# Kernel optimization log

Hardware: AMD Instinct MI355X
Metric: run time of the kernel (lower is better)

## Reference

```python
import jax, jax.numpy as jnp
import numpy as np

B, S, HID = 1, 4096, 1024
NH, HD = 16, 64            # heads, per-head dim
BS = 256                    # block size
PB = 256                    # position buckets (= max_relative_positions)
EPS = 1e-7


def make_log_bucket_position(rel, num_buckets, max_position):
    sign = jnp.sign(rel)
    max_exact = num_buckets // 2
    in_exact = (rel < max_exact) & (rel > -max_exact)
    abs_pos = jnp.where(in_exact, max_exact - 1, jnp.abs(rel))
    x = jnp.log((max_position - 1) / max_exact)
    xx = jnp.log(abs_pos / max_exact) / x
    log_pos = jnp.ceil(xx * (max_exact - 1)) + max_exact
    return jnp.where(abs_pos <= max_exact, rel, (log_pos * sign).astype(jnp.int32)).astype(jnp.int32)


def split_into_blocks(x, block_size, axis):
    # [..., S, ...] -> [..., S//bs, bs, ...]; S assumed divisible by bs
    shp = x.shape
    new = shp[:axis] + (shp[axis] // block_size, block_size) + shp[axis + 1:]
    return x.reshape(new)


def concat_3_blocks(x, block_axis, seq_axis, pad_value=0):
    # pad one zero block on each side of the block axis, then concat
    # [prev, cur, next] along the within-block seq axis.
    pad = [(0, 0)] * x.ndim
    pad[block_axis] = (1, 1)
    xp = jnp.pad(x, pad, constant_values=pad_value)
    nb = x.shape[block_axis]
    slices = [jax.lax.dynamic_slice_in_dim(xp, i, nb, block_axis) for i in range(3)]
    return jnp.concatenate(slices, axis=seq_axis)


def layer_norm(x, scale, bias):
    mu = jnp.mean(x, axis=-1, keepdims=True)
    var = jnp.mean(jnp.square(x - mu), axis=-1, keepdims=True)
    return (x - mu) * jax.lax.rsqrt(var + EPS) * scale + bias


def setup_inputs() -> dict:
    key = jax.random.key(0)
    ks = jax.random.split(key, 8)
    d = {
        'hidden_states': jax.random.normal(ks[0], (B, S, HID), jnp.float32) * 0.02,
        'rel_pos_embeddings': jax.random.normal(ks[1], (S, HID), jnp.float32) * 0.02,
        'Wq': jax.random.normal(ks[2], (HID, HID), jnp.float32) * 0.01,
        'bq': jnp.zeros((HID,), jnp.float32),
        'Wk': jax.random.normal(ks[3], (HID, HID), jnp.float32) * 0.01,
        'bk': jnp.zeros((HID,), jnp.float32),
        'Wv': jax.random.normal(ks[4], (HID, HID), jnp.float32) * 0.01,
        'bv': jnp.zeros((HID,), jnp.float32),
        'Wo': jax.random.normal(ks[5], (HID, HID), jnp.float32) * 0.01,
        'bo': jnp.zeros((HID,), jnp.float32),
        'ln_scale': jnp.ones((HID,), jnp.float32),
        'ln_bias': jnp.zeros((HID,), jnp.float32),
    }
    return d


def reference(hidden_states, rel_pos_embeddings, Wq, bq, Wk, bk, Wv, bv, Wo, bo, ln_scale, ln_bias):
    b, s, hid = hidden_states.shape

    def heads(x):
        return x.reshape(x.shape[:-1] + (NH, HD))

    # content projections -> [B, nb, bs, h, d]
    q = split_into_blocks(heads(hidden_states @ Wq + bq), BS, axis=1)
    k = split_into_blocks(heads(hidden_states @ Wk + bk), BS, axis=1)
    v = split_into_blocks(heads(hidden_states @ Wv + bv), BS, axis=1)
    k3 = concat_3_blocks(k, block_axis=1, seq_axis=2)   # [B, nb, 3bs, h, d]
    v3 = concat_3_blocks(v, block_axis=1, seq_axis=2)

    c2c = jnp.einsum('bnqhd,bnkhd->bnhqk', q, k3)

    # position projections, stacked over batch (size-1 batch dim broadcasts in einsum)
    pos_q = split_into_blocks(heads(rel_pos_embeddings @ Wq + bq)[None], BS, axis=1)  # [1, nb, bs, h, d]
    pos_k = split_into_blocks(heads(rel_pos_embeddings @ Wk + bk)[None], BS, axis=1)
    pos_k3 = concat_3_blocks(pos_k, block_axis=1, seq_axis=2)                          # [1, nb, 3bs, h, d]

    rel = jnp.arange(BS, dtype=jnp.int32)[:, None] - jnp.arange(3 * BS, dtype=jnp.int32)[None, :]
    rel = make_log_bucket_position(rel, PB, PB)
    idx = jnp.clip(rel + PB, 0, 2 * PB - 1)            # [bs, 3bs]

    c2p = jnp.einsum('bnqhd,bnkhd->bnhqk', q, pos_k3)  # [B, nb, h, bs, 3bs]
    # faithful to the source: axis-less jnp.take gathers from the FLATTENED
    # score tensor -> [bs, 3bs] bias broadcast over (batch, block, head)
    c2p_bias = jnp.take(c2p, idx)

    p2c = jnp.einsum('bnqhd,bnkhd->bnhqk', pos_q, k3)
    p2c_bias = jnp.take(p2c, idx)

    scale = jnp.sqrt(jnp.asarray(HD * 3, hidden_states.dtype))
    attn = (c2c + c2p_bias + p2c_bias) / scale
    probs = jax.nn.softmax(attn, axis=-1)

    ctx = jnp.einsum('bnhqk,bnkhd->bnqhd', probs, v3)  # [B, nb, bs, h, d]
    ctx = ctx.reshape(b, s, hid)
    out = ctx @ Wo + bo
    return layer_norm(out + hidden_states, ln_scale, ln_bias)
```

## Files before the change

kernel.cpp:

```cpp
#include <hip/hip_runtime.h>
#include <stdint.h>

typedef unsigned short u16;
typedef __bf16 bf16_t;
typedef bf16_t v8bf __attribute__((ext_vector_type(8)));
typedef float v4f __attribute__((ext_vector_type(4)));

#define SEQ   4096
#define HIDN  1024
#define NHEAD 16
#define HDIM  64
#define BLK   256
#define NBLK  16

#define GLOAD_LDS16(g, l) __builtin_amdgcn_global_load_lds( \
  (const __attribute__((address_space(1))) unsigned*)(g), \
  (__attribute__((address_space(3))) unsigned*)(l), 16, 0, 0)

__device__ __forceinline__ u16 f2bf(float f){
  union { float f; unsigned u; } v; v.f = f;
  unsigned r = (v.u + 0x7fffu + ((v.u >> 16) & 1u)) >> 16;
  return (u16)r;
}
__device__ __forceinline__ float bf2f(u16 h){
  union { unsigned u; float f; } v; v.u = ((unsigned)h) << 16;
  return v.f;
}

__global__ __launch_bounds__(256) void k_prep(const float* __restrict__ hidden, u16* __restrict__ hb,
    const float* __restrict__ Wq, const float* __restrict__ Wk,
    const float* __restrict__ Wv, const float* __restrict__ Wo, u16* __restrict__ Wt,
    const float* __restrict__ bq, const float* __restrict__ bk, const float* __restrict__ bv,
    float* __restrict__ bcat,
    const float* __restrict__ rpe, float* __restrict__ posk, float* __restrict__ posq0)
{
  __shared__ float t[32][33];
  __shared__ float red[4][64];
  int b = blockIdx.x, tid = threadIdx.x;
  if (b < 4096){
    int w = b >> 10, tile = b & 1023;
    int k0 = (tile & 31) * 32, n0 = (tile >> 5) * 32;
    const float* W = (w == 0) ? Wq : (w == 1) ? Wk : (w == 2) ? Wv : Wo;
    u16* outp = Wt + (size_t)w * 1024 * 1024;
    int x = tid & 31, y = tid >> 5;
    #pragma unroll
    for (int yy = 0; yy < 32; yy += 8) t[y + yy][x] = W[(size_t)(k0 + y + yy) * 1024 + n0 + x];
    __syncthreads();
    #pragma unroll
    for (int yy = 0; yy < 32; yy += 8) outp[(size_t)(n0 + y + yy) * 1024 + k0 + x] = f2bf(t[x][y + yy]);
  } else if (b < 4608){
    int base = (b - 4096) * 8192;
    #pragma unroll
    for (int j = 0; j < 8; j++){
      int i = base + j * 1024 + tid * 4;
      float4 f = *(const float4*)&hidden[i];
      unsigned u0 = (unsigned)f2bf(f.x) | ((unsigned)f2bf(f.y) << 16);
      unsigned u1 = (unsigned)f2bf(f.z) | ((unsigned)f2bf(f.w) << 16);
      uint2 p; p.x = u0; p.y = u1;
      *(uint2*)&hb[i] = p;
    }
  } else if (b == 4608){
    #pragma unroll
    for (int j = 0; j < 12; j++){
      int i = j * 256 + tid;
      const float* src = i < 1024 ? bq : (i < 2048 ? bk : bv);
      bcat[i] = src[i & 1023];
    }
  } else {
    int pb = b - 4609;
    int d = tid & 63, part = tid >> 6;
    const float* W  = (pb < 256) ? Wk : Wq;
    const float* rv = (pb < 256) ? &rpe[(size_t)pb * 1024] : rpe;
    float s = 0.f;
    for (int k = part * 256; k < part * 256 + 256; k++) s += rv[k] * W[(size_t)k * 1024 + d];
    red[part][d] = s;
    __syncthreads();
    if (part == 0){
      s = red[0][d] + red[1][d] + red[2][d] + red[3][d];
      if (pb < 256) posk[pb * 64 + d] = s + bk[d];
      else          posq0[d] = s + bq[d];
    }
  }
}

__global__ __launch_bounds__(256) void k_gemm_qkv(const u16* __restrict__ A, const u16* __restrict__ Bt,
                                                  const float* __restrict__ bias,
                                                  u16* __restrict__ qk, u16* __restrict__ Vt)
{
  __shared__ alignas(16) u16 As[2][128 * 32];
  __shared__ alignas(16) u16 Bs[2][128 * 32];
  int tid = threadIdx.x, lane = tid & 63, wid = tid >> 6;
  int wr = wid >> 1, wc = wid & 1;
  int m0 = blockIdx.y * 128, n0 = blockIdx.x * 128;
  const int K = 1024;

  v4f acc[4][4];
  #pragma unroll
  for (int m = 0; m < 4; m++)
    #pragma unroll
    for (int n = 0; n < 4; n++) acc[m][n] = (v4f){0.f, 0.f, 0.f, 0.f};

  int r = lane & 15, g = lane >> 4;
  int ob0 = wid * 2048;
  int o0  = ob0 + lane * 16;
  int row0 = o0 >> 6, col0 = (o0 & 63) >> 1;
  int row1 = (o0 + 1024) >> 6, col1 = ((o0 + 1024) & 63) >> 1;

  GLOAD_LDS16(&A [(size_t)(m0 + row0) * K + col0], &As[0][ob0 >> 1]);
  GLOAD_LDS16(&Bt[(size_t)(n0 + row0) * K + col0], &Bs[0][ob0 >> 1]);
  GLOAD_LDS16(&A [(size_t)(m0 + row1) * K + col1], &As[0][(ob0 + 1024) >> 1]);
  GLOAD_LDS16(&Bt[(size_t)(n0 + row1) * K + col1], &Bs[0][(ob0 + 1024) >> 1]);
  __syncthreads();

  int cur = 0;
  for (int kt = 0; kt < K - 32; kt += 32){
    int nx = cur ^ 1, kn = kt + 32;
    GLOAD_LDS16(&A [(size_t)(m0 + row0) * K + kn + col0], &As[nx][ob0 >> 1]);
    GLOAD_LDS16(&Bt[(size_t)(n0 + row0) * K + kn + col0], &Bs[nx][ob0 >> 1]);
    GLOAD_LDS16(&A [(size_t)(m0 + row1) * K + kn + col1], &As[nx][(ob0 + 1024) >> 1]);
    GLOAD_LDS16(&Bt[(size_t)(n0 + row1) * K + kn + col1], &Bs[nx][(ob0 + 1024) >> 1]);

    v8bf a[4], bb[4];
    #pragma unroll
    for (int m = 0; m < 4; m++) a[m] = *(const v8bf*)&As[cur][(wr * 64 + m * 16 + r) * 32 + g * 8];
    #pragma unroll
    for (int n = 0; n < 4; n++) bb[n] = *(const v8bf*)&Bs[cur][(wc * 64 + n * 16 + r) * 32 + g * 8];
    #pragma unroll
    for (int m = 0; m < 4; m++)
      #pragma unroll
      for (int n = 0; n < 4; n++)
        acc[m][n] = __builtin_amdgcn_mfma_f32_16x16x32_bf16(a[m], bb[n], acc[m][n], 0, 0, 0);
    __syncthreads();
    cur = nx;
  }
  {
    v8bf a[4], bb[4];
    #pragma unroll
    for (int m = 0; m < 4; m++) a[m] = *(const v8bf*)&As[cur][(wr * 64 + m * 16 + r) * 32 + g * 8];
    #pragma unroll
    for (int n = 0; n < 4; n++) bb[n] = *(const v8bf*)&Bs[cur][(wc * 64 + n * 16 + r) * 32 + g * 8];
    #pragma unroll
    for (int m = 0; m < 4; m++)
      #pragma unroll
      for (int n = 0; n < 4; n++)
        acc[m][n] = __builtin_amdgcn_mfma_f32_16x16x32_bf16(a[m], bb[n], acc[m][n], 0, 0, 0);
  }

  #pragma unroll
  for (int m = 0; m < 4; m++)
    #pragma unroll
    for (int n = 0; n < 4; n++){
      int col = n0 + wc * 64 + n * 16 + r;
      float bv = bias[col];
      if (n0 < 2048){
        #pragma unroll
        for (int i = 0; i < 4; i++){
          int row = m0 + wr * 64 + m * 16 + g * 4 + i;
          qk[(size_t)row * 2048 + col] = f2bf(acc[m][n][i] + bv);
        }
      } else {
        unsigned lo = (unsigned)f2bf(acc[m][n][0] + bv) | ((unsigned)f2bf(acc[m][n][1] + bv) << 16);
        unsigned hi = (unsigned)f2bf(acc[m][n][2] + bv) | ((unsigned)f2bf(acc[m][n][3] + bv) << 16);
        uint2 pk; pk.x = lo; pk.y = hi;
        int row = m0 + wr * 64 + m * 16 + g * 4;
        *(uint2*)&Vt[(size_t)(col - 2048) * 4096 + row] = pk;
      }
    }
}

__global__ __launch_bounds__(256) void k_gemm_out(const u16* __restrict__ A, const u16* __restrict__ Bt,
                                                  const float* __restrict__ bias,
                                                  const float* __restrict__ resid, float* __restrict__ Cout)
{
  __shared__ alignas(16) u16 As[2][128 * 32];
  __shared__ alignas(16) u16 Bs[2][128 * 32];
  int tid = threadIdx.x, lane = tid & 63, wid = tid >> 6;
  int wr = wid >> 1, wc = wid & 1;
  int m0 = blockIdx.y * 128, n0 = blockIdx.x * 128;
  const int K = 1024;

  v4f acc[4][4];
  #pragma unroll
  for (int m = 0; m < 4; m++)
    #pragma unroll
    for (int n = 0; n < 4; n++) acc[m][n] = (v4f){0.f, 0.f, 0.f, 0.f};

  int r = lane & 15, g = lane >> 4;
  int ob0 = wid * 2048;
  int o0  = ob0 + lane * 16;
  int row0 = o0 >> 6, col0 = (o0 & 63) >> 1;
  int row1 = (o0 + 1024) >> 6, col1 = ((o0 + 1024) & 63) >> 1;

  GLOAD_LDS16(&A [(size_t)(m0 + row0) * K + col0], &As[0][ob0 >> 1]);
  GLOAD_LDS16(&Bt[(size_t)(n0 + row0) * K + col0], &Bs[0][ob0 >> 1]);
  GLOAD_LDS16(&A [(size_t)(m0 + row1) * K + col1], &As[0][(ob0 + 1024) >> 1]);
  GLOAD_LDS16(&Bt[(size_t)(n0 + row1) * K + col1], &Bs[0][(ob0 + 1024) >> 1]);
  __syncthreads();

  int cur = 0;
  for (int kt = 0; kt < K - 32; kt += 32){
    int nx = cur ^ 1, kn = kt + 32;
    GLOAD_LDS16(&A [(size_t)(m0 + row0) * K + kn + col0], &As[nx][ob0 >> 1]);
    GLOAD_LDS16(&Bt[(size_t)(n0 + row0) * K + kn + col0], &Bs[nx][ob0 >> 1]);
    GLOAD_LDS16(&A [(size_t)(m0 + row1) * K + kn + col1], &As[nx][(ob0 + 1024) >> 1]);
    GLOAD_LDS16(&Bt[(size_t)(n0 + row1) * K + kn + col1], &Bs[nx][(ob0 + 1024) >> 1]);

    v8bf a[4], bb[4];
    #pragma unroll
    for (int m = 0; m < 4; m++) a[m] = *(const v8bf*)&As[cur][(wr * 64 + m * 16 + r) * 32 + g * 8];
    #pragma unroll
    for (int n = 0; n < 4; n++) bb[n] = *(const v8bf*)&Bs[cur][(wc * 64 + n * 16 + r) * 32 + g * 8];
    #pragma unroll
    for (int m = 0; m < 4; m++)
      #pragma unroll
      for (int n = 0; n < 4; n++)
        acc[m][n] = __builtin_amdgcn_mfma_f32_16x16x32_bf16(a[m], bb[n], acc[m][n], 0, 0, 0);
    __syncthreads();
    cur = nx;
  }
  {
    v8bf a[4], bb[4];
    #pragma unroll
    for (int m = 0; m < 4; m++) a[m] = *(const v8bf*)&As[cur][(wr * 64 + m * 16 + r) * 32 + g * 8];
    #pragma unroll
    for (int n = 0; n < 4; n++) bb[n] = *(const v8bf*)&Bs[cur][(wc * 64 + n * 16 + r) * 32 + g * 8];
    #pragma unroll
    for (int m = 0; m < 4; m++)
      #pragma unroll
      for (int n = 0; n < 4; n++)
        acc[m][n] = __builtin_amdgcn_mfma_f32_16x16x32_bf16(a[m], bb[n], acc[m][n], 0, 0, 0);
  }

  #pragma unroll
  for (int m = 0; m < 4; m++)
    #pragma unroll
    for (int n = 0; n < 4; n++){
      int col = n0 + wc * 64 + n * 16 + r;
      float bv = bias[col];
      #pragma unroll
      for (int i = 0; i < 4; i++){
        int row = m0 + wr * 64 + m * 16 + g * 4 + i;
        Cout[(size_t)row * 1024 + col] = acc[m][n][i] + bv + resid[(size_t)row * 1024 + col];
      }
    }
}

__global__ __launch_bounds__(256) void k_brow(const u16* __restrict__ qk,
                                              const float* __restrict__ posk, const float* __restrict__ posq0,
                                              float* __restrict__ brow)
{
  int b = blockIdx.x, tid = threadIdx.x;
  if (tid < 32) brow[b * 32 + tid] = 0.f;
  int u = b * 32 + (tid >> 3), sub = tid & 7;
  float c2p = 0.f, p2c = 0.f;
  #pragma unroll
  for (int j = 0; j < 8; j++){
    int d = sub * 8 + j;
    c2p += bf2f(qk[d]) * posk[u * 64 + d];
    p2c += posq0[d] * bf2f(qk[(size_t)u * 2048 + 1024 + d]);
  }
  float v = c2p + p2c;
  v += __shfl_xor(v, 1);
  v += __shfl_xor(v, 2);
  v += __shfl_xor(v, 4);
  if (sub == 0) brow[256 + u] = v;
}

__global__ void k_biasd(const float* __restrict__ brow, float* __restrict__ biasd)
{
  int t = blockIdx.x * blockDim.x + threadIdx.x;
  int rel = t - 767;
  int bucket;
  bool in_exact = (rel < 128) && (rel > -128);
  int abs_pos = in_exact ? 127 : (rel < 0 ? -rel : rel);
  if (abs_pos <= 128) bucket = rel;
  else {
    float xx = logf((float)abs_pos * (1.0f / 128.0f)) / logf(255.0f / 128.0f);
    float lp = ceilf(xx * 127.0f) + 128.0f;
    int sgn = (rel > 0) ? 1 : ((rel < 0) ? -1 : 0);
    bucket = (int)lp * sgn;
  }
  int idx = bucket + 256;
  idx = idx < 0 ? 0 : (idx > 511 ? 511 : idx);
  biasd[t] = brow[idx];
}

__global__ __launch_bounds__(256) void k_attn(const u16* __restrict__ qk, const u16* __restrict__ Vt,
                                              const float* __restrict__ biasd, u16* __restrict__ ctxg)
{
  __shared__ alignas(16) u16 Ks[128 * 64];
  __shared__ alignas(16) u16 Vs[64 * 128];
  __shared__ alignas(16) u16 Ps[4 * 16 * 128];
  __shared__ float bias_s[1024];

  int b = blockIdx.x;
  int h = b & 15, tile = b >> 4;
  int n = tile >> 2, qb0 = (tile & 3) * 64;
  int tid = threadIdx.x, lane = tid & 63, w = tid >> 6;
  int q0 = tile * 64;
  int g0 = (n - 1) * 256;
  const float c1 = 0.07216878364870323f * 1.4426950408889634f;
  int r = lane & 15, g = lane >> 4;

  *(float4*)&bias_s[tid * 4] = *(const float4*)&biasd[tid * 4];

  v8bf qfrag[2];
  {
    const u16* src = &qk[(size_t)(q0 + w * 16 + r) * 2048 + h * 64 + g * 8];
    qfrag[0] = *(const v8bf*)&src[0];
    qfrag[1] = *(const v8bf*)&src[32];
  }

  u16* Pw = &Ps[w * 2048];
  float m4[4], l4[4];
  v4f pacc[4];
  #pragma unroll
  for (int i = 0; i < 4; i++){ m4[i] = -3.0e38f; l4[i] = 0.f; pacc[i] = (v4f){0.f,0.f,0.f,0.f}; }

  for (int c = 0; c < 6; ++c){
    int cb = g0 + c * 128;
    bool oob = (cb < 0) || (cb >= SEQ);
    if (!oob){
      #pragma unroll
      for (int t = 0; t < 4; ++t){
        int row = w * 32 + t * 8 + (lane >> 3);
        int p = lane & 7;
        GLOAD_LDS16(&qk[(size_t)(cb + row) * 2048 + 1024 + h * 64 + ((p ^ (row & 7)) * 8)],
                    Ks + (size_t)(w * 32 + t * 8) * 64);
      }
      #pragma unroll
      for (int t = 0; t < 4; ++t){
        int d = w * 16 + t * 4 + (lane >> 4);
        int p = lane & 15;
        GLOAD_LDS16(&Vt[(size_t)(h * 64 + d) * 4096 + cb + ((p ^ (d & 7)) * 8)],
                    Vs + (size_t)(w * 16 + t * 4) * 128);
      }
    }
    __syncthreads();

    v4f sacc[8];
    #pragma unroll
    for (int t = 0; t < 8; t++) sacc[t] = (v4f){0.f,0.f,0.f,0.f};
    if (!oob){
      #pragma unroll
      for (int ks = 0; ks < 2; ++ks){
        #pragma unroll
        for (int t = 0; t < 8; t++){
          int kr = t * 16 + r;
          v8bf bb = *(const v8bf*)&Ks[kr * 64 + (((4 * ks + g) ^ (kr & 7)) * 8)];
          sacc[t] = __builtin_amdgcn_mfma_f32_16x16x32_bf16(qfrag[ks], bb, sacc[t], 0, 0, 0);
        }
      }
    }

    float sv[8][4];
    float cm[4] = {-3.0e38f, -3.0e38f, -3.0e38f, -3.0e38f};
    int ib = qb0 + w * 16 + g * 4 + 767 - r - c * 128;
    #pragma unroll
    for (int t = 0; t < 8; t++){
      #pragma unroll
      for (int i = 0; i < 4; i++){
        float s = (sacc[t][i] + bias_s[ib + i - t * 16]) * c1;
        sv[t][i] = s;
        cm[i] = fmaxf(cm[i], s);
      }
    }
    #pragma unroll
    for (int i = 0; i < 4; i++){
      cm[i] = fmaxf(cm[i], __shfl_xor(cm[i], 1));
      cm[i] = fmaxf(cm[i], __shfl_xor(cm[i], 2));
      cm[i] = fmaxf(cm[i], __shfl_xor(cm[i], 4));
      cm[i] = fmaxf(cm[i], __shfl_xor(cm[i], 8));
    }
    #pragma unroll
    for (int i = 0; i < 4; i++){
      float mn = fmaxf(m4[i], cm[i]);
      float sc = exp2f(m4[i] - mn);
      m4[i] = mn;
      l4[i] *= sc;
      #pragma unroll
      for (int nn = 0; nn < 4; nn++) pacc[nn][i] *= sc;
    }
    #pragma unroll
    for (int t = 0; t < 8; t++){
      #pragma unroll
      for (int i = 0; i < 4; i++){
        float p = exp2f(sv[t][i] - m4[i]);
        l4[i] += p;
        if (!oob){
          int row = g * 4 + i;
          Pw[row * 128 + (((2 * t + (r >> 3)) ^ (row & 7)) * 8) + (r & 7)] = f2bf(p);
        }
      }
    }

    if (!oob){
      #pragma unroll
      for (int ks = 0; ks < 4; ++ks){
        v8bf a = *(const v8bf*)&Pw[r * 128 + (((4 * ks + g) ^ (r & 7)) * 8)];
        #pragma unroll
        for (int nn = 0; nn < 4; nn++){
          int d = nn * 16 + r;
          v8bf bb = *(const v8bf*)&Vs[d * 128 + (((4 * ks + g) ^ (d & 7)) * 8)];
          pacc[nn] = __builtin_amdgcn_mfma_f32_16x16x32_bf16(a, bb, pacc[nn], 0, 0, 0);
        }
      }
    }
    __syncthreads();
  }

  float inv4[4];
  #pragma unroll
  for (int i = 0; i < 4; i++){
    l4[i] += __shfl_xor(l4[i], 1);
    l4[i] += __shfl_xor(l4[i], 2);
    l4[i] += __shfl_xor(l4[i], 4);
    l4[i] += __shfl_xor(l4[i], 8);
    inv4[i] = 1.0f / l4[i];
  }
  #pragma unroll
  for (int nn = 0; nn < 4; nn++){
    int d = nn * 16 + r;
    #pragma unroll
    for (int i = 0; i < 4; i++){
      int qrow = q0 + w * 16 + g * 4 + i;
      ctxg[(size_t)qrow * 1024 + h * 64 + d] = f2bf(pacc[nn][i] * inv4[i]);
    }
  }
}

__global__ __launch_bounds__(256) void k_ln(float* __restrict__ out,
                                            const float* __restrict__ gamma, const float* __restrict__ beta)
{
  __shared__ float red[8];
  int row = blockIdx.x, tid = threadIdx.x;
  int lane = tid & 63, wid = tid >> 6;
  size_t base = (size_t)row * 1024 + tid * 4;
  float4 xv = *(const float4*)&out[base];
  float v0 = xv.x, v1 = xv.y, v2 = xv.z, v3 = xv.w;
  float s = v0 + v1 + v2 + v3;
  float q = v0 * v0 + v1 * v1 + v2 * v2 + v3 * v3;
  #pragma unroll
  for (int o = 32; o; o >>= 1){ s += __shfl_down(s, o); q += __shfl_down(q, o); }
  if (lane == 0){ red[wid] = s; red[4 + wid] = q; }
  __syncthreads();
  float ts = red[0] + red[1] + red[2] + red[3];
  float tq = red[4] + red[5] + red[6] + red[7];
  float mu = ts * (1.0f / 1024.0f);
  float var = tq * (1.0f / 1024.0f) - mu * mu;
  float rstd = rsqrtf(var + 1e-7f);
  int c = tid * 4;
  out[base + 0] = (v0 - mu) * rstd * gamma[c + 0] + beta[c + 0];
  out[base + 1] = (v1 - mu) * rstd * gamma[c + 1] + beta[c + 1];
  out[base + 2] = (v2 - mu) * rstd * gamma[c + 2] + beta[c + 2];
  out[base + 3] = (v3 - mu) * rstd * gamma[c + 3] + beta[c + 3];
}

extern "C" void kernel_launch(void* const* d_in, const int* in_sizes, int n_in,
                              void* d_out, int out_size, void* d_ws, size_t ws_size,
                              hipStream_t stream)
{
  const float* hidden = (const float*)d_in[0];
  const float* rpe    = (const float*)d_in[1];
  const float* Wq = (const float*)d_in[2];
  const float* bq = (const float*)d_in[3];
  const float* Wk = (const float*)d_in[4];
  const float* bk = (const float*)d_in[5];
  const float* Wv = (const float*)d_in[6];
  const float* bv = (const float*)d_in[7];
  const float* Wo = (const float*)d_in[8];
  const float* bo = (const float*)d_in[9];
  const float* lns = (const float*)d_in[10];
  const float* lnb = (const float*)d_in[11];
  float* out = (float*)d_out;

  char* ws = (char*)d_ws;
  size_t off = 0;
  auto alloc = [&](size_t bytes){ void* p = ws + off; off += (bytes + 255) & ~(size_t)255; return p; };
  u16* hb      = (u16*)alloc((size_t)SEQ * HIDN * 2);
  u16* Wt      = (u16*)alloc((size_t)4 * HIDN * HIDN * 2);
  u16* qk      = (u16*)alloc((size_t)SEQ * 2048 * 2);
  u16* Vt      = (u16*)alloc((size_t)HIDN * SEQ * 2);
  u16* ctxb    = (u16*)alloc((size_t)SEQ * HIDN * 2);
  float* bcat  = (float*)alloc(3072 * 4);
  float* poskf = (float*)alloc(256 * 64 * 4);
  float* posq0 = (float*)alloc(64 * 4);
  float* brow  = (float*)alloc(512 * 4);
  float* biasd = (float*)alloc(1024 * 4);
  (void)ws_size; (void)in_sizes; (void)n_in; (void)out_size;

  k_prep<<<4866, 256, 0, stream>>>(hidden, hb, Wq, Wk, Wv, Wo, Wt,
                                   bq, bk, bv, bcat, rpe, poskf, posq0);

  k_gemm_qkv<<<dim3(24, 32), 256, 0, stream>>>(hb, Wt, bcat, qk, Vt);

  k_brow<<<8, 256, 0, stream>>>(qk, poskf, posq0, brow);
  k_biasd<<<4, 256, 0, stream>>>(brow, biasd);

  k_attn<<<64 * NHEAD, 256, 0, stream>>>(qk, Vt, biasd, ctxb);

  k_gemm_out<<<dim3(8, 32), 256, 0, stream>>>(ctxb, Wt + (size_t)3 * HIDN * HIDN, bo, hidden, out);

  k_ln<<<SEQ, 256, 0, stream>>>(out, lns, lnb);
}
```

Before: 155.3 us.

## Compute transposed QK^T so softmax probabilities stay in registers, drop LDS P buffer

The attention kernel swaps the MFMA operand order so each lane holds scores for one query row across keys. Row max and sum then need only two cross-lane shuffles instead of four per row. The probability tile is packed to bf16 and rearranged into the PV MFMA A-fragment layout with lane shuffles, removing the shared-memory P buffer and its write/read round trip. In exchange it adds many ds_bpermute shuffles per chunk and per-row broadcasts of the rescale factors, which could offset the LDS savings.

After: 146.7 us. 5.6% less time.

```diff
diff --git a/kernel.cpp b/kernel.cpp
--- a/kernel.cpp
+++ b/kernel.cpp
@@ -25,6 +25,9 @@
 __device__ __forceinline__ float bf2f(u16 h){
   union { unsigned u; float f; } v; v.u = ((unsigned)h) << 16;
   return v.f;
+}
+__device__ __forceinline__ unsigned packbf(float a, float b){
+  return (unsigned)f2bf(a) | ((unsigned)f2bf(b) << 16);
 }
 
 __global__ __launch_bounds__(256) void k_prep(const float* __restrict__ hidden, u16* __restrict__ hb,
@@ -159,8 +162,8 @@
           qk[(size_t)row * 2048 + col] = f2bf(acc[m][n][i] + bv);
         }
       } else {
-        unsigned lo = (unsigned)f2bf(acc[m][n][0] + bv) | ((unsigned)f2bf(acc[m][n][1] + bv) << 16);
-        unsigned hi = (unsigned)f2bf(acc[m][n][2] + bv) | ((unsigned)f2bf(acc[m][n][3] + bv) << 16);
+        unsigned lo = packbf(acc[m][n][0] + bv, acc[m][n][1] + bv);
+        unsigned hi = packbf(acc[m][n][2] + bv, acc[m][n][3] + bv);
         uint2 pk; pk.x = lo; pk.y = hi;
         int row = m0 + wr * 64 + m * 16 + g * 4;
         *(uint2*)&Vt[(size_t)(col - 2048) * 4096 + row] = pk;
@@ -290,7 +293,6 @@
 {
   __shared__ alignas(16) u16 Ks[128 * 64];
   __shared__ alignas(16) u16 Vs[64 * 128];
-  __shared__ alignas(16) u16 Ps[4 * 16 * 128];
   __shared__ float bias_s[1024];
 
   int b = blockIdx.x;
@@ -311,11 +313,14 @@
     qfrag[1] = *(const v8bf*)&src[32];
   }
 
-  u16* Pw = &Ps[w * 2048];
-  float m4[4], l4[4];
+  float mrun = -3.0e38f, lrun = 0.f;
   v4f pacc[4];
   #pragma unroll
-  for (int i = 0; i < 4; i++){ m4[i] = -3.0e38f; l4[i] = 0.f; pacc[i] = (v4f){0.f,0.f,0.f,0.f}; }
+  for (int nn = 0; nn < 4; nn++) pacc[nn] = (v4f){0.f,0.f,0.f,0.f};
+
+  int idxA = r + ((g & 1) << 5);
+  int idxB = idxA + 16;
+  int myrnd = g >> 1;
 
   for (int c = 0; c < 6; ++c){
     int cb = g0 + c * 128;
@@ -347,84 +352,86 @@
         #pragma unroll
         for (int t = 0; t < 8; t++){
           int kr = t * 16 + r;
-          v8bf bb = *(const v8bf*)&Ks[kr * 64 + (((4 * ks + g) ^ (kr & 7)) * 8)];
-          sacc[t] = __builtin_amdgcn_mfma_f32_16x16x32_bf16(qfrag[ks], bb, sacc[t], 0, 0, 0);
+          v8bf kf = *(const v8bf*)&Ks[kr * 64 + (((4 * ks + g) ^ (kr & 7)) * 8)];
+          sacc[t] = __builtin_amdgcn_mfma_f32_16x16x32_bf16(kf, qfrag[ks], sacc[t], 0, 0, 0);
         }
       }
     }
 
     float sv[8][4];
-    float cm[4] = {-3.0e38f, -3.0e38f, -3.0e38f, -3.0e38f};
-    int ib = qb0 + w * 16 + g * 4 + 767 - r - c * 128;
+    float cmax = -3.0e38f;
+    int ib = qb0 + w * 16 + r + 767 - c * 128 - g * 4;
     #pragma unroll
     for (int t = 0; t < 8; t++){
       #pragma unroll
       for (int i = 0; i < 4; i++){
-        float s = (sacc[t][i] + bias_s[ib + i - t * 16]) * c1;
+        float s = (sacc[t][i] + bias_s[ib - t * 16 - i]) * c1;
         sv[t][i] = s;
-        cm[i] = fmaxf(cm[i], s);
-      }
-    }
+        cmax = fmaxf(cmax, s);
+      }
+    }
+    cmax = fmaxf(cmax, __shfl_xor(cmax, 16));
+    cmax = fmaxf(cmax, __shfl_xor(cmax, 32));
+    float mn = fmaxf(mrun, cmax);
+    float sc = exp2f(mrun - mn);
+    mrun = mn;
+    lrun *= sc;
     #pragma unroll
     for (int i = 0; i < 4; i++){
-      cm[i] = fmaxf(cm[i], __shfl_xor(cm[i], 1));
-      cm[i] = fmaxf(cm[i], __shfl_xor(cm[i], 2));
-      cm[i] = fmaxf(cm[i], __shfl_xor(cm[i], 4));
-      cm[i] = fmaxf(cm[i], __shfl_xor(cm[i], 8));
-    }
-    #pragma unroll
-    for (int i = 0; i < 4; i++){
-      float mn = fmaxf(m4[i], cm[i]);
-      float sc = exp2f(m4[i] - mn);
-      m4[i] = mn;
-      l4[i] *= sc;
-      #pragma unroll
-      for (int nn = 0; nn < 4; nn++) pacc[nn][i] *= sc;
-    }
+      float sci = __shfl(sc, (g << 2) + i);
+      #pragma unroll
+      for (int nn = 0; nn < 4; nn++) pacc[nn][i] *= sci;
+    }
+
+    unsigned pk0[8], pk1[8];
     #pragma unroll
     for (int t = 0; t < 8; t++){
-      #pragma unroll
-      for (int i = 0; i < 4; i++){
-        float p = exp2f(sv[t][i] - m4[i]);
-        l4[i] += p;
-        if (!oob){
-          int row = g * 4 + i;
-          Pw[row * 128 + (((2 * t + (r >> 3)) ^ (row & 7)) * 8) + (r & 7)] = f2bf(p);
+      float p0 = exp2f(sv[t][0] - mn);
+      float p1 = exp2f(sv[t][1] - mn);
+      float p2 = exp2f(sv[t][2] - mn);
+      float p3 = exp2f(sv[t][3] - mn);
+      lrun += (p0 + p1) + (p2 + p3);
+      pk0[t] = packbf(p0, p1);
+      pk1[t] = packbf(p2, p3);
+    }
+
+    if (!oob){
+      #pragma unroll
+      for (int bb4 = 0; bb4 < 4; ++bb4){
+        unsigned s0a = 0, s1a = 0, s0b = 0, s1b = 0;
+        #pragma unroll
+        for (int rnd = 0; rnd < 2; ++rnd){
+          int t = 2 * bb4 + rnd;
+          unsigned ta0 = __shfl(pk0[t], idxA);
+          unsigned ta1 = __shfl(pk1[t], idxA);
+          unsigned tb0 = __shfl(pk0[t], idxB);
+          unsigned tb1 = __shfl(pk1[t], idxB);
+          if (myrnd == rnd){ s0a = ta0; s1a = ta1; s0b = tb0; s1b = tb1; }
         }
-      }
-    }
-
-    if (!oob){
-      #pragma unroll
-      for (int ks = 0; ks < 4; ++ks){
-        v8bf a = *(const v8bf*)&Pw[r * 128 + (((4 * ks + g) ^ (r & 7)) * 8)];
+        union { unsigned u[4]; v8bf v; } af;
+        af.u[0] = s0a; af.u[1] = s1a; af.u[2] = s0b; af.u[3] = s1b;
         #pragma unroll
         for (int nn = 0; nn < 4; nn++){
           int d = nn * 16 + r;
-          v8bf bb = *(const v8bf*)&Vs[d * 128 + (((4 * ks + g) ^ (d & 7)) * 8)];
-          pacc[nn] = __builtin_amdgcn_mfma_f32_16x16x32_bf16(a, bb, pacc[nn], 0, 0, 0);
+          v8bf vb = *(const v8bf*)&Vs[d * 128 + (((4 * bb4 + g) ^ (d & 7)) * 8)];
+          pacc[nn] = __builtin_amdgcn_mfma_f32_16x16x32_bf16(af.v, vb, pacc[nn], 0, 0, 0);
         }
       }
     }
     __syncthreads();
   }
 
-  float inv4[4];
-  #pragma unroll
-  for (int i = 0; i < 4; i++){
-    l4[i] += __shfl_xor(l4[i], 1);
-    l4[i] += __shfl_xor(l4[i], 2);
-    l4[i] += __shfl_xor(l4[i], 4);
-    l4[i] += __shfl_xor(l4[i], 8);
-    inv4[i] = 1.0f / l4[i];
-  }
+  lrun += __shfl_xor(lrun, 16);
+  lrun += __shfl_xor(lrun, 32);
+  float inv = 1.0f / lrun;
   #pragma unroll
   for (int nn = 0; nn < 4; nn++){
     int d = nn * 16 + r;
     #pragma unroll
     for (int i = 0; i < 4; i++){
+      float invi = __shfl(inv, (g << 2) + i);
       int qrow = q0 + w * 16 + g * 4 + i;
-      ctxg[(size_t)qrow * 1024 + h * 64 + d] = f2bf(pacc[nn][i] * inv4[i]);
+      ctxg[(size_t)qrow * 1024 + h * 64 + d] = f2bf(pacc[nn][i] * invi);
     }
   }
 }
```
